# Kernel tuning notes

Measured on AMD Instinct MI355X. Metric: run time of the kernel, lower is better.

Reference implementation:

```python
import jax, jax.numpy as jnp
import numpy as np

N_HEAD = 16

def setup_inputs() -> dict:
    key = jax.random.key(0)
    ks = jax.random.split(key, 4)
    B, T, C = 4, 2048, 1024
    x = jax.random.normal(ks[0], (B, T, C), dtype=jnp.float32)
    # causal mask: 1 where attendable (lower triangle), 0 elsewhere
    attn_mask = jnp.tril(jnp.ones((T, T), dtype=jnp.int32))[None, None, :, :]
    s = 0.02
    Wqkv = jax.random.normal(ks[1], (C, 3 * C), dtype=jnp.float32) * s
    bqkv = jnp.zeros((3 * C,), dtype=jnp.float32)
    Wout = jax.random.normal(ks[2], (C, C), dtype=jnp.float32) * s
    bout = jnp.zeros((C,), dtype=jnp.float32)
    return {"x": x, "attn_mask": attn_mask, "Wqkv": Wqkv, "bqkv": bqkv, "Wout": Wout, "bout": bout}

def reference(x, attn_mask, Wqkv, bqkv, Wout, bout):
    B, T, C = x.shape
    H = N_HEAD
    D = C // H
    qkv = x @ Wqkv + bqkv  # [B,T,3C]
    q, k, v = jnp.split(qkv, 3, axis=2)
    # [B,T,C] -> [B,H,T,D]
    q = q.reshape(B, T, H, D).transpose(0, 2, 1, 3)
    k = k.reshape(B, T, H, D).transpose(0, 2, 1, 3)
    v = v.reshape(B, T, H, D).transpose(0, 2, 1, 3)
    scores = jnp.einsum('bhqd,bhkd->bhqk', q, k) / jnp.sqrt(jnp.float32(D))
    scores = jnp.where(attn_mask == 0, jnp.float32(-jnp.inf), scores)
    probs = jax.nn.softmax(scores, axis=-1)  # dropout is identity in eval
    out = jnp.einsum('bhqk,bhkd->bhqd', probs, v)
    out = out.transpose(0, 2, 1, 3).reshape(B, T, C)
    return out @ Wout + bout
```

## Files before the change

kernel.cpp:

```cpp
#include <hip/hip_runtime.h>
#include <hip/hip_bf16.h>
#include <stdint.h>

#define TT 2048
#define CC 1024
#define HH 16
#define DD 64

typedef __bf16 bf16;
typedef bf16 bf16x8 __attribute__((ext_vector_type(8)));
typedef float f32x4 __attribute__((ext_vector_type(4)));
typedef float f32x16 __attribute__((ext_vector_type(16)));
typedef unsigned u32x4 __attribute__((ext_vector_type(4)));
typedef unsigned u32x2 __attribute__((ext_vector_type(2)));

#define MFMA16(a, b, c) __builtin_amdgcn_mfma_f32_16x16x32_bf16(a, b, c, 0, 0, 0)
#define MFMA32(a, b, c) __builtin_amdgcn_mfma_f32_32x32x16_bf16(a, b, c, 0, 0, 0)

#define SCLQ 0.18033688011112043f

typedef __attribute__((address_space(1))) unsigned int u32_g;
typedef __attribute__((address_space(3))) unsigned int u32_l;

__device__ __forceinline__ void gload_lds16(const void* g, void* l) {
  __builtin_amdgcn_global_load_lds((u32_g*)g, (u32_l*)l, 16, 0, 0);
}

__device__ __forceinline__ unsigned cvtpk(float a, float b) {
  unsigned r;
  asm("v_cvt_pk_bf16_f32 %0, %1, %2" : "=v"(r) : "v"(a), "v"(b));
  return r;
}

__device__ __forceinline__ void plswap(unsigned& a, unsigned& b) {
  asm("v_permlane32_swap_b32 %0, %1" : "+v"(a), "+v"(b));
}

__global__ __launch_bounds__(256) void k_cvt(const float* __restrict__ in,
                                             bf16* __restrict__ out, int n8) {
  int i = blockIdx.x * 256 + threadIdx.x;
  if (i >= n8) return;
  const float4* p = (const float4*)in + (size_t)i * 2;
  float4 a = p[0], b = p[1];
  bf16x8 o;
  o[0] = (bf16)a.x; o[1] = (bf16)a.y; o[2] = (bf16)a.z; o[3] = (bf16)a.w;
  o[4] = (bf16)b.x; o[5] = (bf16)b.y; o[6] = (bf16)b.z; o[7] = (bf16)b.w;
  *((bf16x8*)out + i) = o;
}

__global__ __launch_bounds__(256) void k_transpose_w(const float* __restrict__ in,
                                                     bf16* __restrict__ out,
                                                     int R, int C) {
  __shared__ float tile[64][65];
  int tcn = C >> 6;
  int tc = blockIdx.x % tcn;
  int tr = blockIdx.x / tcn;
  int t = threadIdx.x;
  int r0 = t >> 4;
  int cv = t & 15;
  const float4* src = (const float4*)(in + (size_t)(tr * 64) * C + tc * 64);
  int strideV = C >> 2;
#pragma unroll
  for (int p = 0; p < 4; ++p) {
    int r = r0 + p * 16;
    float4 v = src[(size_t)r * strideV + cv];
    tile[r][cv * 4 + 0] = v.x;
    tile[r][cv * 4 + 1] = v.y;
    tile[r][cv * 4 + 2] = v.z;
    tile[r][cv * 4 + 3] = v.w;
  }
  __syncthreads();
  int nn0 = t >> 3;
  int ck = t & 7;
#pragma unroll
  for (int p = 0; p < 2; ++p) {
    int nn = nn0 + p * 32;
    bf16x8 o;
#pragma unroll
    for (int i = 0; i < 8; ++i) o[i] = (bf16)tile[ck * 8 + i][nn];
    *(bf16x8*)(out + (size_t)(tc * 64 + nn) * R + tr * 64 + ck * 8) = o;
  }
}

template <int MODE>
__global__ __launch_bounds__(512) void k_gemm(const bf16* __restrict__ A,
                                              const bf16* __restrict__ Bt,
                                              int Kdim, int N,
                                              const float* __restrict__ bias,
                                              bf16* __restrict__ Qd,
                                              bf16* __restrict__ Kd,
                                              bf16* __restrict__ Vd,
                                              float* __restrict__ Fd) {
  __shared__ __align__(16) char lds[147456];
  int nwg = gridDim.x;
  int bid = blockIdx.x;
  int cpx = nwg >> 3;
  int swz = (bid & 7) * cpx + (bid >> 3);
  int gx = N >> 7;
  int tm = swz / gx, tn = swz % gx;
  int tid = threadIdx.x;
  int wid = tid >> 6, lane = tid & 63;
  int wm = (wid >> 1) * 64;
  int wn = (wid & 1) * 64;

  f32x4 acc[4][4];
#pragma unroll
  for (int i = 0; i < 4; ++i)
#pragma unroll
    for (int j = 0; j < 4; ++j) acc[i][j] = {0.f, 0.f, 0.f, 0.f};

  int srow = tid >> 3;
  int sinn = (((tid & 7) ^ ((tid >> 3) & 7)) << 4) >> 1;
  int ldst = (tid & 7) << 4;
  const bf16* Ab = A + (size_t)(tm * 256 + srow) * Kdim + sinn;
  const bf16* Bb = Bt + (size_t)(tn * 128 + srow) * Kdim + sinn;

  int NTt = Kdim >> 6;

#pragma unroll
  for (int t0 = 0; t0 < 2; ++t0) {
    char* sa = lds + t0 * 49152;
    char* sb = sa + 32768;
    int ks = t0 * 64;
#pragma unroll
    for (int c = 0; c < 4; ++c)
      gload_lds16(Ab + (size_t)(c * 64) * Kdim + ks, sa + c * 8192 + (tid >> 3) * 128 + ldst);
#pragma unroll
    for (int c = 0; c < 2; ++c)
      gload_lds16(Bb + (size_t)(c * 64) * Kdim + ks, sb + c * 8192 + (tid >> 3) * 128 + ldst);
  }

  int fr = lane & 15;
  int fx = ((lane >> 4) * 16) ^ ((lane & 7) << 4);

#pragma unroll 1
  for (int t = 0; t < NTt; ++t) {
    if (t < NTt - 1)
      asm volatile("s_waitcnt vmcnt(6)" ::: "memory");
    else
      asm volatile("s_waitcnt vmcnt(0)" ::: "memory");
    __builtin_amdgcn_sched_barrier(0);
    __builtin_amdgcn_s_barrier();
    __builtin_amdgcn_sched_barrier(0);

    if (t + 2 < NTt) {
      int slot = t + 2;
      while (slot >= 3) slot -= 3;
      char* sa = lds + slot * 49152;
      char* sb = sa + 32768;
      int ks = (t + 2) * 64;
#pragma unroll
      for (int c = 0; c < 4; ++c)
        gload_lds16(Ab + (size_t)(c * 64) * Kdim + ks, sa + c * 8192 + (tid >> 3) * 128 + ldst);
#pragma unroll
      for (int c = 0; c < 2; ++c)
        gload_lds16(Bb + (size_t)(c * 64) * Kdim + ks, sb + c * 8192 + (tid >> 3) * 128 + ldst);
    }

    int cslot = t;
    while (cslot >= 3) cslot -= 3;
    const char* sa = lds + cslot * 49152;
    const char* sb = sa + 32768;
#pragma unroll
    for (int kk = 0; kk < 2; ++kk) {
      bf16x8 af[4], bfv[4];
      int inb = kk * 64;
#pragma unroll
      for (int i = 0; i < 4; ++i) {
        af[i] = *(const bf16x8*)(sa + (wm + i * 16 + fr) * 128 + (inb ^ fx));
        bfv[i] = *(const bf16x8*)(sb + (wn + i * 16 + fr) * 128 + (inb ^ fx));
      }
      __builtin_amdgcn_s_setprio(1);
#pragma unroll
      for (int i = 0; i < 4; ++i)
#pragma unroll
        for (int j = 0; j < 4; ++j) acc[i][j] = MFMA16(af[i], bfv[j], acc[i][j]);
      __builtin_amdgcn_s_setprio(0);
    }
  }

  int r0 = (lane >> 4) * 4;
  int cn = lane & 15;
  if (MODE == 0) {
    int n0 = tn * 128 + wn;
    int which = n0 >> 10;
#pragma unroll
    for (int j = 0; j < 4; ++j) {
      int n = n0 + j * 16 + cn;
      float bv = bias[n];
      int h = (n >> 6) & 15;
      int d = n & 63;
#pragma unroll
      for (int i = 0; i < 4; ++i) {
#pragma unroll
        for (int r = 0; r < 4; ++r) {
          int m = tm * 256 + wm + i * 16 + r0 + r;
          int b = m >> 11, t = m & 2047;
          float val = acc[i][j][r] + bv;
          if (which == 0)
            Qd[(((size_t)(b * HH + h)) * TT + t) * DD + d] = (bf16)(val * SCLQ);
          else if (which == 1)
            Kd[(((size_t)(b * HH + h)) * TT + t) * DD + d] = (bf16)val;
          else
            Vd[(((size_t)(b * HH + h)) * DD + d) * TT + t] = (bf16)val;
        }
      }
    }
  } else {
#pragma unroll
    for (int j = 0; j < 4; ++j) {
      int n = tn * 128 + wn + j * 16 + cn;
      float bv = bias[n];
#pragma unroll
      for (int i = 0; i < 4; ++i) {
#pragma unroll
        for (int r = 0; r < 4; ++r) {
          int m = tm * 256 + wm + i * 16 + r0 + r;
          Fd[(size_t)m * N + n] = acc[i][j][r] + bv;
        }
      }
    }
  }
}

template <bool MASKED>
__device__ __forceinline__ void attn_tile(const char* __restrict__ sK,
                                          const char* __restrict__ sV,
                                          const bf16x8 qf[4],
                                          f32x16& o0, f32x16& o1, float& lrun,
                                          int base0, const int* __restrict__ colp,
                                          int hi, int qabs, int kvb) {
  f32x16 s0, s1;
#pragma unroll
  for (int g = 0; g < 16; ++g) { s0[g] = 0.f; s1[g] = 0.f; }
#pragma unroll
  for (int c = 0; c < 4; ++c) {
    bf16x8 kf0 = *(const bf16x8*)(sK + base0 + colp[c]);
    bf16x8 kf1 = *(const bf16x8*)(sK + base0 + 4096 + colp[c]);
    s0 = MFMA32(kf0, qf[c], s0);
    s1 = MFMA32(kf1, qf[c], s1);
  }
  float rs = 0.f;
#pragma unroll
  for (int g = 0; g < 16; ++g) {
    float p0 = __builtin_amdgcn_exp2f(s0[g]);
    float p1 = __builtin_amdgcn_exp2f(s1[g]);
    if (MASKED) {
      int kvr = (g & 3) + 8 * (g >> 2) + 4 * hi;
      p0 = (kvb + kvr <= qabs) ? p0 : 0.f;
      p1 = (kvb + 32 + kvr <= qabs) ? p1 : 0.f;
    }
    s0[g] = p0; s1[g] = p1;
    rs += p0 + p1;
  }
  lrun += rs;

  unsigned pk[8], qk[8];
#pragma unroll
  for (int i = 0; i < 8; ++i) {
    pk[i] = cvtpk(s0[2 * i], s0[2 * i + 1]);
    qk[i] = cvtpk(s1[2 * i], s1[2 * i + 1]);
  }
  plswap(pk[0], pk[2]); plswap(pk[1], pk[3]);
  plswap(pk[4], pk[6]); plswap(pk[5], pk[7]);
  plswap(qk[0], qk[2]); plswap(qk[1], qk[3]);
  plswap(qk[4], qk[6]); plswap(qk[5], qk[7]);

  bf16x8 pfr[4];
  pfr[0] = __builtin_bit_cast(bf16x8, (u32x4){pk[0], pk[1], pk[2], pk[3]});
  pfr[1] = __builtin_bit_cast(bf16x8, (u32x4){pk[4], pk[5], pk[6], pk[7]});
  pfr[2] = __builtin_bit_cast(bf16x8, (u32x4){qk[0], qk[1], qk[2], qk[3]});
  pfr[3] = __builtin_bit_cast(bf16x8, (u32x4){qk[4], qk[5], qk[6], qk[7]});

#pragma unroll
  for (int cc = 0; cc < 4; ++cc) {
    bf16x8 vf0 = *(const bf16x8*)(sV + base0 + colp[cc]);
    bf16x8 vf1 = *(const bf16x8*)(sV + base0 + 4096 + colp[cc]);
    o0 = MFMA32(vf0, pfr[cc], o0);
    o1 = MFMA32(vf1, pfr[cc], o1);
  }
}

__global__ __launch_bounds__(256) void k_attn(const bf16* __restrict__ Qg,
                                              const bf16* __restrict__ Kg,
                                              const bf16* __restrict__ Vtg,
                                              bf16* __restrict__ O) {
  __shared__ __align__(16) char lds[32768];

  int bid = blockIdx.x;
  int bh = (bid & 7) * 8 + ((bid >> 3) & 7);
  int pair = bid >> 6;
  int wid = threadIdx.x >> 6, lane = threadIdx.x & 63;
  int l31 = lane & 31, hi = lane >> 5;

  const bf16* Qh = Qg + (size_t)bh * TT * DD;
  const bf16* Kh = Kg + (size_t)bh * TT * DD;
  const bf16* Vh = Vtg + (size_t)bh * DD * TT;

  int base0 = l31 * 128;
  int colp[4];
#pragma unroll
  for (int c = 0; c < 4; ++c) colp[c] = (32 * c + 16 * hi) ^ ((l31 & 7) << 4);

  int soff[2], srow[2], scol[2];
#pragma unroll
  for (int c = 0; c < 2; ++c) {
    int off = (wid * 2 + c) * 1024 + lane * 16;
    soff[c] = (wid * 2 + c) * 1024;
    srow[c] = off >> 7;
    scol[c] = (off & 127) ^ ((srow[c] & 7) << 4);
  }

  int b = bh >> 4, h = bh & 15;

#pragma unroll 1
  for (int half = 0; half < 2; ++half) {
    int qt = half ? (15 - pair) : pair;
    int qb = qt * 128;
    int qw = qb + wid * 32;
    int qabs = qw + l31;

    bf16x8 qf[4];
#pragma unroll
    for (int c = 0; c < 4; ++c)
      qf[c] = *(const bf16x8*)(Qh + (size_t)qabs * DD + c * 16 + hi * 8);

    f32x16 o0, o1;
#pragma unroll
    for (int g = 0; g < 16; ++g) { o0[g] = 0.f; o1[g] = 0.f; }
    float lrun = 0.f;

    int ntile = 2 * qt + 2;

#pragma unroll
    for (int c = 0; c < 2; ++c) {
      gload_lds16(Kh + (size_t)srow[c] * DD + (scol[c] >> 1), lds + soff[c]);
      gload_lds16(Vh + (size_t)srow[c] * TT + (scol[c] >> 1), lds + 8192 + soff[c]);
    }
    __syncthreads();

    int cur = 0;
    for (int tk = 0; tk < ntile; ++tk) {
      int kvb = tk * 64;
      if (tk + 1 < ntile) {
        int kvn = kvb + 64;
        char* dK = lds + (cur ^ 1) * 16384;
        char* dV = dK + 8192;
#pragma unroll
        for (int c = 0; c < 2; ++c) {
          gload_lds16(Kh + (size_t)(kvn + srow[c]) * DD + (scol[c] >> 1), dK + soff[c]);
          gload_lds16(Vh + (size_t)srow[c] * TT + kvn + (scol[c] >> 1), dV + soff[c]);
        }
      }
      const char* sK = lds + cur * 16384;
      const char* sV = sK + 8192;
      if (kvb + 63 <= qw)
        attn_tile<false>(sK, sV, qf, o0, o1, lrun, base0, colp, hi, qabs, kvb);
      else if (kvb <= qw + 31)
        attn_tile<true>(sK, sV, qf, o0, o1, lrun, base0, colp, hi, qabs, kvb);
      __syncthreads();
      cur ^= 1;
    }

    lrun += __shfl_xor(lrun, 32);
    float rl = 1.0f / lrun;
    bf16* baseO = O + ((size_t)(b * TT + qabs)) * CC + h * 64;
#pragma unroll
    for (int G = 0; G < 4; ++G) {
      unsigned w0 = cvtpk(o0[4 * G] * rl, o0[4 * G + 1] * rl);
      unsigned w1 = cvtpk(o0[4 * G + 2] * rl, o0[4 * G + 3] * rl);
      *(u32x2*)(baseO + 8 * G + 4 * hi) = (u32x2){w0, w1};
      unsigned w2 = cvtpk(o1[4 * G] * rl, o1[4 * G + 1] * rl);
      unsigned w3 = cvtpk(o1[4 * G + 2] * rl, o1[4 * G + 3] * rl);
      *(u32x2*)(baseO + 32 + 8 * G + 4 * hi) = (u32x2){w2, w3};
    }
  }
}

extern "C" void kernel_launch(void* const* d_in, const int* in_sizes, int n_in,
                              void* d_out, int out_size, void* d_ws, size_t ws_size,
                              hipStream_t stream) {
  const float* x = (const float*)d_in[0];
  const float* Wqkv = (const float*)d_in[2];
  const float* bqkv = (const float*)d_in[3];
  const float* Wout = (const float*)d_in[4];
  const float* bout = (const float*)d_in[5];
  float* out = (float*)d_out;

  char* ws = (char*)d_ws;
  bf16* xb  = (bf16*)(ws);
  bf16* wt1 = (bf16*)(ws + (16u << 20));
  bf16* wt2 = (bf16*)(ws + (22u << 20));
  bf16* Qb  = (bf16*)(ws + (24u << 20));
  bf16* Kb  = (bf16*)(ws + (40u << 20));
  bf16* Vt  = (bf16*)(ws + (56u << 20));
  bf16* Ob  = (bf16*)(ws + (72u << 20));

  k_cvt<<<4096, 256, 0, stream>>>(x, xb, (4 * TT * CC) / 8);
  k_transpose_w<<<768, 256, 0, stream>>>(Wqkv, wt1, 1024, 3072);
  k_transpose_w<<<256, 256, 0, stream>>>(Wout, wt2, 1024, 1024);
  k_gemm<0><<<768, 512, 0, stream>>>(xb, wt1, 1024, 3072, bqkv, Qb, Kb, Vt, nullptr);
  k_attn<<<512, 256, 0, stream>>>(Qb, Kb, Vt, Ob);
  k_gemm<1><<<256, 512, 0, stream>>>(Ob, wt2, 1024, 1024, bout, nullptr, nullptr, nullptr, out);
}
```

Before: 271.3 us.

## Enlarge GEMM tiles to 256x256 with K=32 stages and XCD-aware tile mapping

The GEMM block tile grows from 256x128 to 256x256. Each wave now computes 128x64 with 8x4 MFMA accumulators, and the K-step drops from 64 to 32 with a new row-pair XOR swizzle and precomputed LDS fragment offsets. Block-to-tile mapping is changed so each XCD owns contiguous M rows, and grid sizes are halved. The aim is better operand reuse and L2 locality, at the cost of more accumulator registers and fewer workgroups (384 and 128 on 256 CUs), which may leave CUs idle and lower occupancy.

Result: slower. 291.6 us (+7.5%).

```diff
diff --git a/kernel.cpp b/kernel.cpp
--- a/kernel.cpp
+++ b/kernel.cpp
@@ -91,98 +91,107 @@
                                               bf16* __restrict__ Kd,
                                               bf16* __restrict__ Vd,
                                               float* __restrict__ Fd) {
-  __shared__ __align__(16) char lds[147456];
-  int nwg = gridDim.x;
+  __shared__ __align__(16) char lds[98304];
+  int gx = N >> 8;
   int bid = blockIdx.x;
-  int cpx = nwg >> 3;
-  int swz = (bid & 7) * cpx + (bid >> 3);
-  int gx = N >> 7;
-  int tm = swz / gx, tn = swz % gx;
+  int xcd = bid & 7;
+  int idx = bid >> 3;
+  int half = idx / (2 * gx);
+  int t2 = idx % (2 * gx);
+  int tn = t2 >> 1;
+  int tm = xcd * 4 + half * 2 + (t2 & 1);
+
   int tid = threadIdx.x;
   int wid = tid >> 6, lane = tid & 63;
-  int wm = (wid >> 1) * 64;
-  int wn = (wid & 1) * 64;
-
-  f32x4 acc[4][4];
-#pragma unroll
-  for (int i = 0; i < 4; ++i)
+  int wm = (wid >> 2) * 128;
+  int wn = (wid & 3) * 64;
+
+  f32x4 acc[8][4];
+#pragma unroll
+  for (int i = 0; i < 8; ++i)
 #pragma unroll
     for (int j = 0; j < 4; ++j) acc[i][j] = {0.f, 0.f, 0.f, 0.f};
 
-  int srow = tid >> 3;
-  int sinn = (((tid & 7) ^ ((tid >> 3) & 7)) << 4) >> 1;
-  int ldst = (tid & 7) << 4;
-  const bf16* Ab = A + (size_t)(tm * 256 + srow) * Kdim + sinn;
-  const bf16* Bb = Bt + (size_t)(tn * 128 + srow) * Kdim + sinn;
-
-  int NTt = Kdim >> 6;
+  int srow[2], ssrc[2], sdst[2];
+#pragma unroll
+  for (int c = 0; c < 2; ++c) {
+    srow[c] = c * 128 + (tid >> 2);
+    ssrc[c] = (((tid & 3) ^ ((srow[c] >> 1) & 3)) << 3);
+    sdst[c] = c * 8192 + tid * 16;
+  }
+  const bf16* Abase = A + (size_t)(tm * 256) * Kdim;
+  const bf16* Bbase = Bt + (size_t)(tn * 256) * Kdim;
+
+  int NT = Kdim >> 5;
 
 #pragma unroll
   for (int t0 = 0; t0 < 2; ++t0) {
-    char* sa = lds + t0 * 49152;
-    char* sb = sa + 32768;
-    int ks = t0 * 64;
-#pragma unroll
-    for (int c = 0; c < 4; ++c)
-      gload_lds16(Ab + (size_t)(c * 64) * Kdim + ks, sa + c * 8192 + (tid >> 3) * 128 + ldst);
-#pragma unroll
-    for (int c = 0; c < 2; ++c)
-      gload_lds16(Bb + (size_t)(c * 64) * Kdim + ks, sb + c * 8192 + (tid >> 3) * 128 + ldst);
+    char* sa = lds + t0 * 32768;
+    char* sb = sa + 16384;
+    int ks = t0 * 32;
+#pragma unroll
+    for (int c = 0; c < 2; ++c) {
+      gload_lds16(Abase + (size_t)srow[c] * Kdim + ks + ssrc[c], sa + sdst[c]);
+      gload_lds16(Bbase + (size_t)srow[c] * Kdim + ks + ssrc[c], sb + sdst[c]);
+    }
   }
 
   int fr = lane & 15;
-  int fx = ((lane >> 4) * 16) ^ ((lane & 7) << 4);
-
+  int abyte[8], bbyte[4];
+#pragma unroll
+  for (int i = 0; i < 8; ++i) {
+    int ra = wm + i * 16 + fr;
+    abyte[i] = ra * 64 + ((((lane >> 4) ^ ((ra >> 1) & 3))) << 4);
+  }
+#pragma unroll
+  for (int j = 0; j < 4; ++j) {
+    int rb = wn + j * 16 + fr;
+    bbyte[j] = rb * 64 + ((((lane >> 4) ^ ((rb >> 1) & 3))) << 4);
+  }
+
+  int cs = 0, ps = 2;
 #pragma unroll 1
-  for (int t = 0; t < NTt; ++t) {
-    if (t < NTt - 1)
-      asm volatile("s_waitcnt vmcnt(6)" ::: "memory");
+  for (int t = 0; t < NT; ++t) {
+    if (t < NT - 1)
+      asm volatile("s_waitcnt vmcnt(4)" ::: "memory");
     else
       asm volatile("s_waitcnt vmcnt(0)" ::: "memory");
-    __builtin_amdgcn_sched_barrier(0);
     __builtin_amdgcn_s_barrier();
     __builtin_amdgcn_sched_barrier(0);
 
-    if (t + 2 < NTt) {
-      int slot = t + 2;
-      while (slot >= 3) slot -= 3;
-      char* sa = lds + slot * 49152;
-      char* sb = sa + 32768;
-      int ks = (t + 2) * 64;
-#pragma unroll
-      for (int c = 0; c < 4; ++c)
-        gload_lds16(Ab + (size_t)(c * 64) * Kdim + ks, sa + c * 8192 + (tid >> 3) * 128 + ldst);
-#pragma unroll
-      for (int c = 0; c < 2; ++c)
-        gload_lds16(Bb + (size_t)(c * 64) * Kdim + ks, sb + c * 8192 + (tid >> 3) * 128 + ldst);
-    }
-
-    int cslot = t;
-    while (cslot >= 3) cslot -= 3;
-    const char* sa = lds + cslot * 49152;
-    const char* sb = sa + 32768;
-#pragma unroll
-    for (int kk = 0; kk < 2; ++kk) {
-      bf16x8 af[4], bfv[4];
-      int inb = kk * 64;
-#pragma unroll
-      for (int i = 0; i < 4; ++i) {
-        af[i] = *(const bf16x8*)(sa + (wm + i * 16 + fr) * 128 + (inb ^ fx));
-        bfv[i] = *(const bf16x8*)(sb + (wn + i * 16 + fr) * 128 + (inb ^ fx));
+    if (t + 2 < NT) {
+      char* sa = lds + ps * 32768;
+      char* sb = sa + 16384;
+      int ks = (t + 2) * 32;
+#pragma unroll
+      for (int c = 0; c < 2; ++c) {
+        gload_lds16(Abase + (size_t)srow[c] * Kdim + ks + ssrc[c], sa + sdst[c]);
+        gload_lds16(Bbase + (size_t)srow[c] * Kdim + ks + ssrc[c], sb + sdst[c]);
       }
-      __builtin_amdgcn_s_setprio(1);
-#pragma unroll
-      for (int i = 0; i < 4; ++i)
-#pragma unroll
-        for (int j = 0; j < 4; ++j) acc[i][j] = MFMA16(af[i], bfv[j], acc[i][j]);
-      __builtin_amdgcn_s_setprio(0);
-    }
+    }
+
+    const char* sa = lds + cs * 32768;
+    const char* sb = sa + 16384;
+    bf16x8 af[8], bfv[4];
+#pragma unroll
+    for (int j = 0; j < 4; ++j) bfv[j] = *(const bf16x8*)(sb + bbyte[j]);
+#pragma unroll
+    for (int i = 0; i < 8; ++i) af[i] = *(const bf16x8*)(sa + abyte[i]);
+    __builtin_amdgcn_s_setprio(1);
+#pragma unroll
+    for (int i = 0; i < 8; ++i)
+#pragma unroll
+      for (int j = 0; j < 4; ++j) acc[i][j] = MFMA16(af[i], bfv[j], acc[i][j]);
+    __builtin_amdgcn_s_setprio(0);
+
+    cs = (cs == 2) ? 0 : cs + 1;
+    ps = (ps == 2) ? 0 : ps + 1;
   }
 
   int r0 = (lane >> 4) * 4;
   int cn = lane & 15;
   if (MODE == 0) {
-    int n0 = tn * 128 + wn;
+    int n0 = tn * 256 + wn;
     int which = n0 >> 10;
 #pragma unroll
     for (int j = 0; j < 4; ++j) {
@@ -191,7 +200,7 @@
       int h = (n >> 6) & 15;
       int d = n & 63;
 #pragma unroll
-      for (int i = 0; i < 4; ++i) {
+      for (int i = 0; i < 8; ++i) {
 #pragma unroll
         for (int r = 0; r < 4; ++r) {
           int m = tm * 256 + wm + i * 16 + r0 + r;
@@ -209,10 +218,10 @@
   } else {
 #pragma unroll
     for (int j = 0; j < 4; ++j) {
-      int n = tn * 128 + wn + j * 16 + cn;
+      int n = tn * 256 + wn + j * 16 + cn;
       float bv = bias[n];
 #pragma unroll
-      for (int i = 0; i < 4; ++i) {
+      for (int i = 0; i < 8; ++i) {
 #pragma unroll
         for (int r = 0; r < 4; ++r) {
           int m = tm * 256 + wm + i * 16 + r0 + r;
@@ -399,7 +408,7 @@
   k_cvt<<<4096, 256, 0, stream>>>(x, xb, (4 * TT * CC) / 8);
   k_transpose_w<<<768, 256, 0, stream>>>(Wqkv, wt1, 1024, 3072);
   k_transpose_w<<<256, 256, 0, stream>>>(Wout, wt2, 1024, 1024);
-  k_gemm<0><<<768, 512, 0, stream>>>(xb, wt1, 1024, 3072, bqkv, Qb, Kb, Vt, nullptr);
+  k_gemm<0><<<384, 512, 0, stream>>>(xb, wt1, 1024, 3072, bqkv, Qb, Kb, Vt, nullptr);
   k_attn<<<512, 256, 0, stream>>>(Qb, Kb, Vt, Ob);
-  k_gemm<1><<<256, 512, 0, stream>>>(Ob, wt2, 1024, 1024, bout, nullptr, nullptr, nullptr, out);
-}
+  k_gemm<1><<<128, 512, 0, stream>>>(Ob, wt2, 1024, 1024, bout, nullptr, nullptr, nullptr, out);
+}
```
